# Kernel optimization log

Measured on AMD Instinct MI355X. Metric: run time of the kernel, lower is better.

Reference implementation:

```python
import jax, jax.numpy as jnp
import numpy as np

NEG_INF = 1e20  # matches INF in the torch source
EPS = 1e-12     # F.normalize default eps
THRESHOLD = 0.1  # config.graph_learn_epsilon_label2label


def setup_inputs() -> dict:
    key = jax.random.key(0)
    k1, k2, k3, k4, k5 = jax.random.split(key, 5)
    L, E, E_PT, H = 2048, 512, 300, 16
    return {
        "label_embedding": jax.random.normal(k1, (L, E), dtype=jnp.float32),
        "pretrained_label_embedding": jax.random.normal(k2, (L, E_PT), dtype=jnp.float32),
        "W_pt": jax.random.normal(k3, (H, E_PT), dtype=jnp.float32) * 0.1,
        "W_gcn0": jax.random.normal(k4, (E, E), dtype=jnp.float32) * (1.0 / np.sqrt(E)),
        "W_gcn1": jax.random.normal(k5, (E, E), dtype=jnp.float32) * (1.0 / np.sqrt(E)),
    }


def _weighted_cosine(input_pt, W_pt):
    # W_pt: [H, E_pt]; input_pt: [L, E_pt]
    w2 = W_pt ** 2                                  # [H, E_pt]
    h = input_pt[None, :, :] * w2[:, None, :]       # [H, L, E_pt]
    norm = jnp.linalg.norm(h, axis=-1, keepdims=True)
    h_norm = h / jnp.maximum(norm, EPS)             # F.normalize(p=2, dim=-1)
    # mean over heads of per-head cosine similarity: [L, L]
    scores = jnp.einsum("hle,hme->hlm", h_norm, h_norm).mean(axis=0)
    return scores


def reference(label_embedding, pretrained_label_embedding, W_pt, W_gcn0, W_gcn1):
    # 1) metric-based graph structure learning
    scores_cosine = _weighted_cosine(pretrained_label_embedding, W_pt)
    scores = jnp.where(scores_cosine >= THRESHOLD, scores_cosine, -NEG_INF)
    adj = jax.nn.softmax(scores, axis=-1)           # [L, L]

    # 2) 2-layer GCN message passing (bias=None, batch_norm=False, eval-mode dropout)
    x = jax.nn.relu(adj @ (label_embedding @ W_gcn0))
    x = jax.nn.relu(adj @ (x @ W_gcn1))
    return x
```

## Files before the change

kernel.cpp:

```cpp
#include <hip/hip_runtime.h>
#include <hip/hip_bf16.h>


typedef __attribute__((ext_vector_type(8))) short bf16x8;
typedef __attribute__((ext_vector_type(4))) float f32x4;
typedef __attribute__((ext_vector_type(4))) int i32x4;

#define L_DIM 2048
#define EPT 300
#define H_DIM 16
#define KDIM 4800
#define WINDOW 3.0e-3f

__global__ __launch_bounds__(256) void compute_y_kernel(const float* __restrict__ xpt,
                                                        const float* __restrict__ Wpt,
                                                        signed char* __restrict__ Y,
                                                        float* __restrict__ norms,
                                                        float* __restrict__ inv_s) {
  __shared__ float redmax[4];
  const int i = blockIdx.x;
  const int lane = threadIdx.x & 63;
  const int w = threadIdx.x >> 6;
  const float* x = xpt + i * EPT;
  float y[4][5];
  float wmax = 0.f;
#pragma unroll
  for (int hh = 0; hh < 4; ++hh) {
    const int h = w * 4 + hh;
    const float* wp = Wpt + h * EPT;
    float ss = 0.f;
#pragma unroll
    for (int t = 0; t < 5; ++t) {
      int e = lane + 64 * t;
      float val = 0.f;
      if (e < EPT) {
        float we = wp[e];
        val = x[e] * we * we;
      }
      y[hh][t] = val;
      ss += val * val;
    }
#pragma unroll
    for (int o = 32; o >= 1; o >>= 1) ss += __shfl_xor(ss, o, 64);
    float n = fmaxf(sqrtf(ss), 1e-12f);
    if (lane == 0) norms[i * H_DIM + h] = n;
    float scale = 0.25f / n;
#pragma unroll
    for (int t = 0; t < 5; ++t) {
      y[hh][t] *= scale;
      wmax = fmaxf(wmax, fabsf(y[hh][t]));
    }
  }
#pragma unroll
  for (int o = 32; o >= 1; o >>= 1) wmax = fmaxf(wmax, __shfl_xor(wmax, o, 64));
  if (lane == 0) redmax[w] = wmax;
  __syncthreads();
  float rowmax = fmaxf(fmaxf(redmax[0], redmax[1]), fmaxf(redmax[2], redmax[3]));
  rowmax = fmaxf(rowmax, 1e-12f);
  const float qs = 127.0f / rowmax;
  if (threadIdx.x == 0) inv_s[i] = rowmax * (1.0f / 127.0f);
#pragma unroll
  for (int hh = 0; hh < 4; ++hh) {
    const int h = w * 4 + hh;
#pragma unroll
    for (int t = 0; t < 5; ++t) {
      int e = lane + 64 * t;
      if (e < EPT) {
        int qv = __float2int_rn(y[hh][t] * qs);
        qv = max(-127, min(127, qv));
        Y[(size_t)i * KDIM + h * EPT + e] = (signed char)qv;
      }
    }
  }
}

__global__ __launch_bounds__(256) void gram_i8(const signed char* __restrict__ Y,
                                               float* __restrict__ S,
                                               const float* __restrict__ inv_s) {
  const int id = blockIdx.x;
  const int bx = (id & 7) | (((id >> 3) & 3) << 3);
  const int by = id >> 5;
  const int row0 = by * 64, col0 = bx * 64;
  if (col0 + 64 <= row0) return;
  const bool do_mirror = (col0 > row0);
  __shared__ __attribute__((aligned(16))) signed char As[4][4096];
  __shared__ __attribute__((aligned(16))) signed char Bs[4][4096];
  const int tid = threadIdx.x;
  const int lane = tid & 63;
  const int wn = tid >> 6;
  const int r = lane & 15, q = lane >> 4;
  const int srow = tid >> 2;
  const int sc = (tid & 3) ^ ((srow >> 2) & 3);

  i32x4 acc[4];
#pragma unroll
  for (int t = 0; t < 4; ++t) {
    i32x4 z = {0, 0, 0, 0};
    acc[t] = z;
  }
  const int niter = KDIM / 64;

#define STAGEI(bufi, k0)                                                                       \
  {                                                                                            \
    __builtin_amdgcn_global_load_lds(                                                          \
        (const __attribute__((address_space(1))) void*)(Y + (size_t)(row0 + srow) * KDIM +     \
                                                        (k0) + sc * 16),                       \
        (__attribute__((address_space(3))) void*)(&As[bufi][tid * 16]), 16, 0, 0);             \
    __builtin_amdgcn_global_load_lds(                                                          \
        (const __attribute__((address_space(1))) void*)(Y + (size_t)(col0 + srow) * KDIM +     \
                                                        (k0) + sc * 16),                       \
        (__attribute__((address_space(3))) void*)(&Bs[bufi][tid * 16]), 16, 0, 0);             \
  }

  auto compute = [&](int bufi) {
    const signed char* as = As[bufi];
    const signed char* bs = Bs[bufi];
    const int ch = (q ^ ((r >> 2) & 3)) * 16;
    i32x4 bfrag = *(const i32x4*)(bs + (wn * 16 + r) * 64 + ch);
#pragma unroll
    for (int t = 0; t < 4; ++t) {
      i32x4 afrag = *(const i32x4*)(as + (t * 16 + r) * 64 + ch);
      acc[t] = __builtin_amdgcn_mfma_i32_16x16x64_i8(afrag, bfrag, acc[t], 0, 0, 0);
    }
  };

  STAGEI(0, 0)
  STAGEI(1, 64)
  STAGEI(2, 128)
  for (int k = 0; k < niter - 3; ++k) {
    asm volatile("s_waitcnt vmcnt(4)" ::: "memory");
    __builtin_amdgcn_s_barrier();
    __builtin_amdgcn_sched_barrier(0);
    STAGEI((k + 3) & 3, (k + 3) * 64)
    compute(k & 3);
  }
  asm volatile("s_waitcnt vmcnt(4)" ::: "memory");
  __builtin_amdgcn_s_barrier();
  __builtin_amdgcn_sched_barrier(0);
  compute((niter - 3) & 3);
  asm volatile("s_waitcnt vmcnt(2)" ::: "memory");
  __builtin_amdgcn_s_barrier();
  __builtin_amdgcn_sched_barrier(0);
  compute((niter - 2) & 3);
  asm volatile("s_waitcnt vmcnt(0)" ::: "memory");
  __builtin_amdgcn_s_barrier();
  __builtin_amdgcn_sched_barrier(0);
  compute((niter - 1) & 3);
#undef STAGEI
  const int gc = col0 + wn * 16 + r;
  const float sj = inv_s[gc];
#pragma unroll
  for (int t = 0; t < 4; ++t) {
    int gr0 = row0 + t * 16 + q * 4;
#pragma unroll
    for (int p = 0; p < 4; ++p) {
      float vv = (float)acc[t][p] * (inv_s[gr0 + p] * sj);
      S[(size_t)(gr0 + p) * L_DIM + gc] = vv;
      if (do_mirror) S[(size_t)gc * L_DIM + (gr0 + p)] = vv;
    }
  }
}

template <int BM, int BN, bool RELU, bool OUT_BF16, bool MIRROR, bool SPLITX>
__global__ __launch_bounds__(256) void gemm_bt(const __hip_bfloat16* __restrict__ A,
                                               const __hip_bfloat16* __restrict__ B,
                                               void* __restrict__ C0v, void* __restrict__ C1v,
                                               int M, int N, int K) {
  constexpr int WMG = BM / 64;
  constexpr int WNG = 4 / WMG;
  constexpr int NC = BN / (16 * WNG);
  int bx = blockIdx.x;
  int kbeg = 0, kend = K;
  if (SPLITX) {
    const int xhalf = gridDim.x >> 1;
    const int khalf = ((K >> 1) + 63) & ~63;
    if (bx >= xhalf) {
      bx -= xhalf;
      kbeg = khalf;
    } else {
      kend = khalf;
    }
  }
  const int row0 = blockIdx.y * BM, col0 = bx * BN;
  if (MIRROR && col0 + BN <= row0) return;
  const bool do_mirror = MIRROR && (col0 > row0);
  __shared__ __attribute__((aligned(16))) __hip_bfloat16 As[2][BM * 64];
  __shared__ __attribute__((aligned(16))) __hip_bfloat16 Bs[2][BN * 64];
  const int tid = threadIdx.x;
  const int lane = tid & 63;
  const int wave = tid >> 6;
  const int wm = wave / WNG, wn = wave % WNG;
  const int r = lane & 15, q = lane >> 4;
  const int srow = tid >> 3;
  const int schunk = (tid & 7) ^ (srow & 7);

  f32x4 acc[4][NC];
#pragma unroll
  for (int a = 0; a < 4; ++a)
#pragma unroll
    for (int b = 0; b < NC; ++b) {
      f32x4 z = {0.f, 0.f, 0.f, 0.f};
      acc[a][b] = z;
    }

  const int niter = (kend - kbeg) >> 6;

#define STAGE(bufi, k0)                                                                       \
  {                                                                                           \
    _Pragma("unroll") for (int it = 0; it < BM / 32; ++it) {                                  \
      __builtin_amdgcn_global_load_lds(                                                       \
          (const __attribute__((address_space(1))) void*)(A + (size_t)(row0 + it * 32 + srow) * K + \
                                                          (k0) + schunk * 8),                 \
          (__attribute__((address_space(3))) void*)(&As[bufi][(it * 256 + tid) * 8]), 16, 0, 0); \
    }                                                                                         \
    _Pragma("unroll") for (int it = 0; it < BN / 32; ++it) {                                  \
      __builtin_amdgcn_global_load_lds(                                                       \
          (const __attribute__((address_space(1))) void*)(B + (size_t)(col0 + it * 32 + srow) * K + \
                                                          (k0) + schunk * 8),                 \
          (__attribute__((address_space(3))) void*)(&Bs[bufi][(it * 256 + tid) * 8]), 16, 0, 0); \
    }                                                                                         \
  }

  STAGE(0, kbeg)
  for (int k = 0; k < niter; ++k) {
    __syncthreads();
    if (k + 1 < niter) STAGE((k + 1) & 1, kbeg + ((k + 1) << 6))
    const __hip_bfloat16* as = As[k & 1];
    const __hip_bfloat16* bs = Bs[k & 1];
#pragma unroll
    for (int kk = 0; kk < 2; ++kk) {
      const int ch = ((kk * 4 + q) ^ (r & 7)) * 8;
      bf16x8 af[4], bfr[NC];
#pragma unroll
      for (int t = 0; t < 4; ++t)
        af[t] = *(const bf16x8*)(as + (wm * 64 + t * 16 + r) * 64 + ch);
#pragma unroll
      for (int c = 0; c < NC; ++c)
        bfr[c] = *(const bf16x8*)(bs + (wn * 16 * NC + c * 16 + r) * 64 + ch);
#pragma unroll
      for (int tm = 0; tm < 4; ++tm)
#pragma unroll
        for (int tn = 0; tn < NC; ++tn)
          acc[tm][tn] = __builtin_amdgcn_mfma_f32_16x16x32_bf16(af[tm], bfr[tn], acc[tm][tn], 0, 0, 0);
    }
  }
#undef STAGE
  float* dst = (float*)(SPLITX ? (kbeg > 0 ? C1v : C0v) : C0v);
#pragma unroll
  for (int tm = 0; tm < 4; ++tm) {
    int gr0 = row0 + wm * 64 + tm * 16 + q * 4;
#pragma unroll
    for (int tn = 0; tn < NC; ++tn) {
      int gc = col0 + wn * 16 * NC + tn * 16 + r;
#pragma unroll
      for (int p = 0; p < 4; ++p) {
        float vv = acc[tm][tn][p];
        if (RELU) vv = fmaxf(vv, 0.f);
        if (OUT_BF16) {
          ((__hip_bfloat16*)C0v)[(size_t)(gr0 + p) * N + gc] = __float2bfloat16(vv);
        } else {
          dst[(size_t)(gr0 + p) * N + gc] = vv;
          if (do_mirror) dst[(size_t)gc * N + (gr0 + p)] = vv;
        }
      }
    }
  }
}

__global__ __launch_bounds__(256) void scan_repair(float* __restrict__ S,
                                                   const float* __restrict__ xpt,
                                                   const float* __restrict__ Wpt,
                                                   const float* __restrict__ norms) {
  __shared__ int lqueue[2048];
  __shared__ int lcount;
  __shared__ float W4[KDIM];
  if (threadIdx.x == 0) lcount = 0;
  __syncthreads();
  const int row = blockIdx.x;
  const int base_idx = row * 2048;
#pragma unroll
  for (int t = 0; t < 2; ++t) {
    int col = t * 1024 + threadIdx.x * 4;
    if (col + 4 <= row) continue;
    float4 v = *(const float4*)(S + base_idx + col);
    float vv[4] = {v.x, v.y, v.z, v.w};
#pragma unroll
    for (int u = 0; u < 4; ++u) {
      int j = col + u;
      if (j >= row && fabsf(vv[u] - 0.1f) < WINDOW) {
        int p = atomicAdd(&lcount, 1);
        if (p < 2048) lqueue[p] = j;
      }
    }
  }
  __syncthreads();
  const int n = min(lcount, 2048);
  if (n == 0) return;
  for (int e = threadIdx.x; e < KDIM; e += 256) {
    float w = Wpt[e];
    float w2 = w * w;
    W4[e] = w2 * w2;
  }
  __syncthreads();
  const int lane = threadIdx.x & 63;
  const int wave = threadIdx.x >> 6;
  const int i = row;
  float xiv[5];
  {
    const float* xi = xpt + i * EPT;
#pragma unroll
    for (int t = 0; t < 5; ++t) {
      int idx = lane + 64 * t;
      xiv[t] = idx < EPT ? xi[idx] : 0.f;
    }
  }
  for (int k = wave; k < n; k += 4) {
    int j = lqueue[k];
    const float* xj = xpt + j * EPT;
    float pre[5];
#pragma unroll
    for (int t = 0; t < 5; ++t) {
      int idx = lane + 64 * t;
      pre[t] = idx < EPT ? xiv[t] * xj[idx] : 0.f;
    }
    float accv = 0.f;
#pragma unroll
    for (int h = 0; h < H_DIM; ++h) {
      float ph = 0.f;
#pragma unroll
      for (int t = 0; t < 5; ++t) {
        int idx = lane + 64 * t;
        if (idx < EPT) ph += pre[t] * W4[h * EPT + idx];
      }
      accv += ph * (1.f / (norms[i * H_DIM + h] * norms[j * H_DIM + h]));
    }
#pragma unroll
    for (int o = 32; o >= 1; o >>= 1) accv += __shfl_xor(accv, o, 64);
    if (lane == 0) {
      float val = accv * (1.f / 16.f);
      S[(size_t)i * L_DIM + j] = val;
      S[(size_t)j * L_DIM + i] = val;
    }
  }
}

__global__ __launch_bounds__(256) void post_kernel(const float* __restrict__ S,
                                                   __hip_bfloat16* __restrict__ adj,
                                                   const float* __restrict__ label,
                                                   __hip_bfloat16* __restrict__ Lbf,
                                                   const float* __restrict__ W0,
                                                   const float* __restrict__ W1,
                                                   __hip_bfloat16* __restrict__ W0t,
                                                   __hip_bfloat16* __restrict__ W1t) {
  __shared__ float red[4];
  __shared__ float tile[32][33];
  const int b = blockIdx.x;
  const int tid = threadIdx.x;
  if (b < 2048) {
    const int row = b;
    const float* s = S + (size_t)row * L_DIM;
    float m = -1e30f;
    for (int j = tid; j < L_DIM; j += 256) {
      float v = s[j];
      if (v >= 0.1f && v > m) m = v;
    }
#pragma unroll
    for (int o = 32; o >= 1; o >>= 1) m = fmaxf(m, __shfl_xor(m, o, 64));
    if ((tid & 63) == 0) red[tid >> 6] = m;
    __syncthreads();
    m = fmaxf(fmaxf(red[0], red[1]), fmaxf(red[2], red[3]));
    float sum = 0.f;
    for (int j = tid; j < L_DIM; j += 256) {
      float v = s[j];
      if (v >= 0.1f) sum += __expf(v - m);
    }
#pragma unroll
    for (int o = 32; o >= 1; o >>= 1) sum += __shfl_xor(sum, o, 64);
    __syncthreads();
    if ((tid & 63) == 0) red[tid >> 6] = sum;
    __syncthreads();
    sum = red[0] + red[1] + red[2] + red[3];
    float inv = 1.f / sum;
    for (int j = tid; j < L_DIM; j += 256) {
      float v = s[j];
      float a = (v >= 0.1f) ? __expf(v - m) * inv : 0.f;
      adj[(size_t)row * L_DIM + j] = __float2bfloat16(a);
    }
    return;
  }
  if (b < 6144) {
    int i = (b - 2048) * 256 + tid;
    Lbf[i] = __float2bfloat16(label[i]);
    return;
  }
  int local = b - 6144;
  const bool first = local < 256;
  const float* src = first ? W0 : W1;
  __hip_bfloat16* dst = first ? W0t : W1t;
  int rem = local & 255;
  int c0 = (rem & 15) * 32, r0 = (rem >> 4) * 32;
  int tx = tid & 31, ty = tid >> 5;
  for (int i2 = ty; i2 < 32; i2 += 8) tile[i2][tx] = src[(size_t)(r0 + i2) * 512 + c0 + tx];
  __syncthreads();
  for (int i2 = ty; i2 < 32; i2 += 8)
    dst[(size_t)(c0 + i2) * 512 + r0 + tx] = __float2bfloat16(tile[tx][i2]);
}

__global__ void combine_relu_bf16(const float* __restrict__ P0, const float* __restrict__ P1,
                                  __hip_bfloat16* __restrict__ X) {
  int i = blockIdx.x * 256 + threadIdx.x;
  float4 a = ((const float4*)P0)[i];
  float4 b = ((const float4*)P1)[i];
  __hip_bfloat16 o0 = __float2bfloat16(fmaxf(a.x + b.x, 0.f));
  __hip_bfloat16 o1 = __float2bfloat16(fmaxf(a.y + b.y, 0.f));
  __hip_bfloat16 o2 = __float2bfloat16(fmaxf(a.z + b.z, 0.f));
  __hip_bfloat16 o3 = __float2bfloat16(fmaxf(a.w + b.w, 0.f));
  X[4 * i + 0] = o0;
  X[4 * i + 1] = o1;
  X[4 * i + 2] = o2;
  X[4 * i + 3] = o3;
}

__global__ void combine_relu_f32(const float* __restrict__ P0, const float* __restrict__ P1,
                                 float* __restrict__ X) {
  int i = blockIdx.x * 256 + threadIdx.x;
  float4 a = ((const float4*)P0)[i];
  float4 b = ((const float4*)P1)[i];
  float4 v;
  v.x = fmaxf(a.x + b.x, 0.f);
  v.y = fmaxf(a.y + b.y, 0.f);
  v.z = fmaxf(a.z + b.z, 0.f);
  v.w = fmaxf(a.w + b.w, 0.f);
  ((float4*)X)[i] = v;
}

extern "C" void kernel_launch(void* const* d_in, const int* in_sizes, int n_in, void* d_out,
                              int out_size, void* d_ws, size_t ws_size, hipStream_t stream) {
  const float* label = (const float*)d_in[0];
  const float* xpt = (const float*)d_in[1];
  const float* Wpt = (const float*)d_in[2];
  const float* W0 = (const float*)d_in[3];
  const float* W1 = (const float*)d_in[4];
  float* out = (float*)d_out;

  char* ws = (char*)d_ws;
  signed char* Y = (signed char*)ws;
  float* S = (float*)(ws + 19660800);
  float* norms = (float*)(ws + 36438016);
  float* P0 = (float*)(ws + 36569088);
  float* P1 = (float*)(ws + 40763392);
  float* inv_s = (float*)(ws + 44957696);
  __hip_bfloat16* adj = (__hip_bfloat16*)ws;
  __hip_bfloat16* Lbf = (__hip_bfloat16*)(ws + 8388608);
  __hip_bfloat16* W0t = (__hip_bfloat16*)(ws + 10485760);
  __hip_bfloat16* W1t = (__hip_bfloat16*)(ws + 11010048);
  __hip_bfloat16* T0t = (__hip_bfloat16*)(ws + 11534336);
  __hip_bfloat16* X1 = (__hip_bfloat16*)(ws + 13631488);
  __hip_bfloat16* T1t = (__hip_bfloat16*)(ws + 15728640);

  compute_y_kernel<<<2048, 256, 0, stream>>>(xpt, Wpt, Y, norms, inv_s);
  gram_i8<<<1024, 256, 0, stream>>>(Y, S, inv_s);
  scan_repair<<<2048, 256, 0, stream>>>(S, xpt, Wpt, norms);
  post_kernel<<<6656, 256, 0, stream>>>(S, adj, label, Lbf, W0, W1, W0t, W1t);
  gemm_bt<64, 64, false, true, false, false><<<dim3(32, 8), 256, 0, stream>>>(W0t, Lbf, T0t, nullptr, 512, 2048, 512);
  gemm_bt<64, 64, false, false, false, true><<<dim3(16, 32), 256, 0, stream>>>(adj, T0t, P0, P1, 2048, 512, 2048);
  combine_relu_bf16<<<1024, 256, 0, stream>>>(P0, P1, X1);
  gemm_bt<64, 64, false, true, false, false><<<dim3(32, 8), 256, 0, stream>>>(W1t, X1, T1t, nullptr, 512, 2048, 512);
  gemm_bt<64, 64, false, false, false, true><<<dim3(16, 32), 256, 0, stream>>>(adj, T1t, P0, P1, 2048, 512, 2048);
  combine_relu_f32<<<1024, 256, 0, stream>>>(P0, P1, out);
}
```

Before: 204.5 us.

## Fuse prep, repair and softmax kernels; drop split-K GEMMs and combine passes

The bf16 casts and weight transposes move into the Y-quantization kernel. The first projection GEMM (W0t x Lbf) now runs on the otherwise idle lower-triangle blocks of the int8 Gram kernel. The near-threshold repair scan merges with the softmax row kernel, which stages the row in LDS and recomputes borderline entries locally instead of writing them back to S. The adjacency GEMMs drop split-K and the separate combine_relu kernels, applying ReLU in-kernel with fewer blocks, which trades parallelism for fewer launches and less traffic.

After: 225.8 us. 10.4% more time.

```diff
diff --git a/kernel.cpp b/kernel.cpp
--- a/kernel.cpp
+++ b/kernel.cpp
@@ -12,83 +12,175 @@
 #define KDIM 4800
 #define WINDOW 3.0e-3f
 
-__global__ __launch_bounds__(256) void compute_y_kernel(const float* __restrict__ xpt,
-                                                        const float* __restrict__ Wpt,
-                                                        signed char* __restrict__ Y,
-                                                        float* __restrict__ norms,
-                                                        float* __restrict__ inv_s) {
+__global__ __launch_bounds__(256) void prep_kernel(const float* __restrict__ xpt,
+                                                   const float* __restrict__ Wpt,
+                                                   const float* __restrict__ label,
+                                                   const float* __restrict__ W0,
+                                                   const float* __restrict__ W1,
+                                                   signed char* __restrict__ Y,
+                                                   float* __restrict__ norms,
+                                                   float* __restrict__ inv_s,
+                                                   __hip_bfloat16* __restrict__ Lbf,
+                                                   __hip_bfloat16* __restrict__ W0t,
+                                                   __hip_bfloat16* __restrict__ W1t) {
   __shared__ float redmax[4];
-  const int i = blockIdx.x;
-  const int lane = threadIdx.x & 63;
-  const int w = threadIdx.x >> 6;
-  const float* x = xpt + i * EPT;
-  float y[4][5];
-  float wmax = 0.f;
-#pragma unroll
-  for (int hh = 0; hh < 4; ++hh) {
-    const int h = w * 4 + hh;
-    const float* wp = Wpt + h * EPT;
-    float ss = 0.f;
-#pragma unroll
-    for (int t = 0; t < 5; ++t) {
-      int e = lane + 64 * t;
-      float val = 0.f;
-      if (e < EPT) {
-        float we = wp[e];
-        val = x[e] * we * we;
-      }
-      y[hh][t] = val;
-      ss += val * val;
-    }
-#pragma unroll
-    for (int o = 32; o >= 1; o >>= 1) ss += __shfl_xor(ss, o, 64);
-    float n = fmaxf(sqrtf(ss), 1e-12f);
-    if (lane == 0) norms[i * H_DIM + h] = n;
-    float scale = 0.25f / n;
-#pragma unroll
-    for (int t = 0; t < 5; ++t) {
-      y[hh][t] *= scale;
-      wmax = fmaxf(wmax, fabsf(y[hh][t]));
-    }
-  }
-#pragma unroll
-  for (int o = 32; o >= 1; o >>= 1) wmax = fmaxf(wmax, __shfl_xor(wmax, o, 64));
-  if (lane == 0) redmax[w] = wmax;
-  __syncthreads();
-  float rowmax = fmaxf(fmaxf(redmax[0], redmax[1]), fmaxf(redmax[2], redmax[3]));
-  rowmax = fmaxf(rowmax, 1e-12f);
-  const float qs = 127.0f / rowmax;
-  if (threadIdx.x == 0) inv_s[i] = rowmax * (1.0f / 127.0f);
-#pragma unroll
-  for (int hh = 0; hh < 4; ++hh) {
-    const int h = w * 4 + hh;
-#pragma unroll
-    for (int t = 0; t < 5; ++t) {
-      int e = lane + 64 * t;
-      if (e < EPT) {
-        int qv = __float2int_rn(y[hh][t] * qs);
-        qv = max(-127, min(127, qv));
-        Y[(size_t)i * KDIM + h * EPT + e] = (signed char)qv;
-      }
-    }
-  }
+  __shared__ float tile[32][33];
+  const int b = blockIdx.x;
+  const int tid = threadIdx.x;
+  if (b < 2048) {
+    const int i = b;
+    const int lane = tid & 63;
+    const int w = tid >> 6;
+    const float* x = xpt + i * EPT;
+    float y[4][5];
+    float wmax = 0.f;
+#pragma unroll
+    for (int hh = 0; hh < 4; ++hh) {
+      const int h = w * 4 + hh;
+      const float* wp = Wpt + h * EPT;
+      float ss = 0.f;
+#pragma unroll
+      for (int t = 0; t < 5; ++t) {
+        int e = lane + 64 * t;
+        float val = 0.f;
+        if (e < EPT) {
+          float we = wp[e];
+          val = x[e] * we * we;
+        }
+        y[hh][t] = val;
+        ss += val * val;
+      }
+#pragma unroll
+      for (int o = 32; o >= 1; o >>= 1) ss += __shfl_xor(ss, o, 64);
+      float n = fmaxf(sqrtf(ss), 1e-12f);
+      if (lane == 0) norms[i * H_DIM + h] = n;
+      float scale = 0.25f / n;
+#pragma unroll
+      for (int t = 0; t < 5; ++t) {
+        y[hh][t] *= scale;
+        wmax = fmaxf(wmax, fabsf(y[hh][t]));
+      }
+    }
+#pragma unroll
+    for (int o = 32; o >= 1; o >>= 1) wmax = fmaxf(wmax, __shfl_xor(wmax, o, 64));
+    if (lane == 0) redmax[w] = wmax;
+    __syncthreads();
+    float rowmax = fmaxf(fmaxf(redmax[0], redmax[1]), fmaxf(redmax[2], redmax[3]));
+    rowmax = fmaxf(rowmax, 1e-12f);
+    const float qs = 127.0f / rowmax;
+    if (tid == 0) inv_s[i] = rowmax * (1.0f / 127.0f);
+#pragma unroll
+    for (int hh = 0; hh < 4; ++hh) {
+      const int h = w * 4 + hh;
+#pragma unroll
+      for (int t = 0; t < 5; ++t) {
+        int e = lane + 64 * t;
+        if (e < EPT) {
+          int qv = __float2int_rn(y[hh][t] * qs);
+          qv = max(-127, min(127, qv));
+          Y[(size_t)i * KDIM + h * EPT + e] = (signed char)qv;
+        }
+      }
+    }
+    return;
+  }
+  if (b < 6144) {
+    int i = (b - 2048) * 256 + tid;
+    Lbf[i] = __float2bfloat16(label[i]);
+    return;
+  }
+  int local = b - 6144;
+  const bool first = local < 256;
+  const float* src = first ? W0 : W1;
+  __hip_bfloat16* dst = first ? W0t : W1t;
+  int rem = local & 255;
+  int c0 = (rem & 15) * 32, r0 = (rem >> 4) * 32;
+  int tx = tid & 31, ty = tid >> 5;
+  for (int i2 = ty; i2 < 32; i2 += 8) tile[i2][tx] = src[(size_t)(r0 + i2) * 512 + c0 + tx];
+  __syncthreads();
+  for (int i2 = ty; i2 < 32; i2 += 8)
+    dst[(size_t)(c0 + i2) * 512 + r0 + tx] = __float2bfloat16(tile[tx][i2]);
 }
 
 __global__ __launch_bounds__(256) void gram_i8(const signed char* __restrict__ Y,
                                                float* __restrict__ S,
-                                               const float* __restrict__ inv_s) {
+                                               const float* __restrict__ inv_s,
+                                               const __hip_bfloat16* __restrict__ W0t,
+                                               const __hip_bfloat16* __restrict__ Lbf,
+                                               __hip_bfloat16* __restrict__ T0t) {
+  __shared__ __attribute__((aligned(16))) char smem[32768];
   const int id = blockIdx.x;
   const int bx = (id & 7) | (((id >> 3) & 3) << 3);
   const int by = id >> 5;
   const int row0 = by * 64, col0 = bx * 64;
-  if (col0 + 64 <= row0) return;
-  const bool do_mirror = (col0 > row0);
-  __shared__ __attribute__((aligned(16))) signed char As[4][4096];
-  __shared__ __attribute__((aligned(16))) signed char Bs[4][4096];
   const int tid = threadIdx.x;
   const int lane = tid & 63;
   const int wn = tid >> 6;
   const int r = lane & 15, q = lane >> 4;
+
+  if (col0 + 64 <= row0) {
+    const int d = (by * (by - 1)) / 2 + bx;
+    if (d >= 256) return;
+    const int row0r = (d >> 5) * 64;
+    const int col0r = (d & 31) * 64;
+    __hip_bfloat16* Asb = (__hip_bfloat16*)smem;
+    __hip_bfloat16* Bsb = (__hip_bfloat16*)(smem + 16384);
+    const int srow8 = tid >> 3;
+    const int schunk8 = (tid & 7) ^ (srow8 & 7);
+    f32x4 racc[4];
+#pragma unroll
+    for (int t = 0; t < 4; ++t) {
+      f32x4 z = {0.f, 0.f, 0.f, 0.f};
+      racc[t] = z;
+    }
+#define RSTAGE(bufi, k0)                                                                      \
+  {                                                                                           \
+    _Pragma("unroll") for (int it = 0; it < 2; ++it) {                                        \
+      __builtin_amdgcn_global_load_lds(                                                       \
+          (const __attribute__((address_space(1))) void*)(W0t + (size_t)(row0r + it * 32 + srow8) * 512 + \
+                                                          (k0) + schunk8 * 8),                \
+          (__attribute__((address_space(3))) void*)(Asb + (bufi)*4096 + (it * 256 + tid) * 8), 16, 0, 0); \
+    }                                                                                         \
+    _Pragma("unroll") for (int it = 0; it < 2; ++it) {                                        \
+      __builtin_amdgcn_global_load_lds(                                                       \
+          (const __attribute__((address_space(1))) void*)(Lbf + (size_t)(col0r + it * 32 + srow8) * 512 + \
+                                                          (k0) + schunk8 * 8),                \
+          (__attribute__((address_space(3))) void*)(Bsb + (bufi)*4096 + (it * 256 + tid) * 8), 16, 0, 0); \
+    }                                                                                         \
+  }
+    RSTAGE(0, 0)
+    for (int k = 0; k < 8; ++k) {
+      __syncthreads();
+      if (k + 1 < 8) RSTAGE((k + 1) & 1, (k + 1) * 64)
+      const __hip_bfloat16* as = Asb + (k & 1) * 4096;
+      const __hip_bfloat16* bs = Bsb + (k & 1) * 4096;
+#pragma unroll
+      for (int kk = 0; kk < 2; ++kk) {
+        const int ch = ((kk * 4 + q) ^ (r & 7)) * 8;
+        bf16x8 af[4];
+#pragma unroll
+        for (int t = 0; t < 4; ++t) af[t] = *(const bf16x8*)(as + (t * 16 + r) * 64 + ch);
+        bf16x8 bfr = *(const bf16x8*)(bs + (wn * 16 + r) * 64 + ch);
+#pragma unroll
+        for (int t = 0; t < 4; ++t)
+          racc[t] = __builtin_amdgcn_mfma_f32_16x16x32_bf16(af[t], bfr, racc[t], 0, 0, 0);
+      }
+    }
+#undef RSTAGE
+    const int gcr = col0r + wn * 16 + r;
+#pragma unroll
+    for (int t = 0; t < 4; ++t) {
+      int gr0 = row0r + t * 16 + q * 4;
+#pragma unroll
+      for (int p = 0; p < 4; ++p)
+        T0t[(size_t)(gr0 + p) * 2048 + gcr] = __float2bfloat16(racc[t][p]);
+    }
+    return;
+  }
+
+  const bool do_mirror = (col0 > row0);
+  signed char* As = (signed char*)smem;
+  signed char* Bs = (signed char*)(smem + 16384);
   const int srow = tid >> 2;
   const int sc = (tid & 3) ^ ((srow >> 2) & 3);
 
@@ -105,16 +197,16 @@
     __builtin_amdgcn_global_load_lds(                                                          \
         (const __attribute__((address_space(1))) void*)(Y + (size_t)(row0 + srow) * KDIM +     \
                                                         (k0) + sc * 16),                       \
-        (__attribute__((address_space(3))) void*)(&As[bufi][tid * 16]), 16, 0, 0);             \
+        (__attribute__((address_space(3))) void*)(As + (bufi)*4096 + tid * 16), 16, 0, 0);     \
     __builtin_amdgcn_global_load_lds(                                                          \
         (const __attribute__((address_space(1))) void*)(Y + (size_t)(col0 + srow) * KDIM +     \
                                                         (k0) + sc * 16),                       \
-        (__attribute__((address_space(3))) void*)(&Bs[bufi][tid * 16]), 16, 0, 0);             \
+        (__attribute__((address_space(3))) void*)(Bs + (bufi)*4096 + tid * 16), 16, 0, 0);     \
   }
 
   auto compute = [&](int bufi) {
-    const signed char* as = As[bufi];
-    const signed char* bs = Bs[bufi];
+    const signed char* as = As + bufi * 4096;
+    const signed char* bs = Bs + bufi * 4096;
     const int ch = (q ^ ((r >> 2) & 3)) * 16;
     i32x4 bfrag = *(const i32x4*)(bs + (wn * 16 + r) * 64 + ch);
 #pragma unroll
@@ -161,29 +253,15 @@
   }
 }
 
-template <int BM, int BN, bool RELU, bool OUT_BF16, bool MIRROR, bool SPLITX>
+template <int BM, int BN, bool RELU, bool OUT_BF16>
 __global__ __launch_bounds__(256) void gemm_bt(const __hip_bfloat16* __restrict__ A,
                                                const __hip_bfloat16* __restrict__ B,
-                                               void* __restrict__ C0v, void* __restrict__ C1v,
+                                               void* __restrict__ C0v,
                                                int M, int N, int K) {
   constexpr int WMG = BM / 64;
   constexpr int WNG = 4 / WMG;
   constexpr int NC = BN / (16 * WNG);
-  int bx = blockIdx.x;
-  int kbeg = 0, kend = K;
-  if (SPLITX) {
-    const int xhalf = gridDim.x >> 1;
-    const int khalf = ((K >> 1) + 63) & ~63;
-    if (bx >= xhalf) {
-      bx -= xhalf;
-      kbeg = khalf;
-    } else {
-      kend = khalf;
-    }
-  }
-  const int row0 = blockIdx.y * BM, col0 = bx * BN;
-  if (MIRROR && col0 + BN <= row0) return;
-  const bool do_mirror = MIRROR && (col0 > row0);
+  const int row0 = blockIdx.y * BM, col0 = blockIdx.x * BN;
   __shared__ __attribute__((aligned(16))) __hip_bfloat16 As[2][BM * 64];
   __shared__ __attribute__((aligned(16))) __hip_bfloat16 Bs[2][BN * 64];
   const int tid = threadIdx.x;
@@ -203,7 +281,7 @@
       acc[a][b] = z;
     }
 
-  const int niter = (kend - kbeg) >> 6;
+  const int niter = K >> 6;
 
 #define STAGE(bufi, k0)                                                                       \
   {                                                                                           \
@@ -221,10 +299,10 @@
     }                                                                                         \
   }
 
-  STAGE(0, kbeg)
+  STAGE(0, 0)
   for (int k = 0; k < niter; ++k) {
     __syncthreads();
-    if (k + 1 < niter) STAGE((k + 1) & 1, kbeg + ((k + 1) << 6))
+    if (k + 1 < niter) STAGE((k + 1) & 1, (k + 1) << 6)
     const __hip_bfloat16* as = As[k & 1];
     const __hip_bfloat16* bs = Bs[k & 1];
 #pragma unroll
@@ -245,7 +323,6 @@
     }
   }
 #undef STAGE
-  float* dst = (float*)(SPLITX ? (kbeg > 0 ? C1v : C0v) : C0v);
 #pragma unroll
   for (int tm = 0; tm < 4; ++tm) {
     int gr0 = row0 + wm * 64 + tm * 16 + q * 4;
@@ -259,179 +336,113 @@
         if (OUT_BF16) {
           ((__hip_bfloat16*)C0v)[(size_t)(gr0 + p) * N + gc] = __float2bfloat16(vv);
         } else {
-          dst[(size_t)(gr0 + p) * N + gc] = vv;
-          if (do_mirror) dst[(size_t)gc * N + (gr0 + p)] = vv;
+          ((float*)C0v)[(size_t)(gr0 + p) * N + gc] = vv;
         }
       }
     }
   }
 }
 
-__global__ __launch_bounds__(256) void scan_repair(float* __restrict__ S,
+__global__ __launch_bounds__(256) void post_kernel(const float* __restrict__ S,
+                                                   __hip_bfloat16* __restrict__ adj,
                                                    const float* __restrict__ xpt,
                                                    const float* __restrict__ Wpt,
                                                    const float* __restrict__ norms) {
-  __shared__ int lqueue[2048];
+  __shared__ float rowv[L_DIM];
+  __shared__ float W4[KDIM];
+  __shared__ int lq[2048];
   __shared__ int lcount;
-  __shared__ float W4[KDIM];
-  if (threadIdx.x == 0) lcount = 0;
-  __syncthreads();
-  const int row = blockIdx.x;
-  const int base_idx = row * 2048;
-#pragma unroll
-  for (int t = 0; t < 2; ++t) {
-    int col = t * 1024 + threadIdx.x * 4;
-    if (col + 4 <= row) continue;
-    float4 v = *(const float4*)(S + base_idx + col);
+  __shared__ float red[4];
+  const int b = blockIdx.x;
+  const int tid = threadIdx.x;
+  if (tid == 0) lcount = 0;
+  __syncthreads();
+  const float* s = S + (size_t)b * L_DIM;
+  for (int j0 = tid * 4; j0 < L_DIM; j0 += 1024) {
+    float4 v = *(const float4*)(s + j0);
+    *(float4*)(&rowv[j0]) = v;
     float vv[4] = {v.x, v.y, v.z, v.w};
 #pragma unroll
     for (int u = 0; u < 4; ++u) {
-      int j = col + u;
-      if (j >= row && fabsf(vv[u] - 0.1f) < WINDOW) {
+      if (fabsf(vv[u] - 0.1f) < WINDOW) {
         int p = atomicAdd(&lcount, 1);
-        if (p < 2048) lqueue[p] = j;
-      }
-    }
-  }
-  __syncthreads();
-  const int n = min(lcount, 2048);
-  if (n == 0) return;
-  for (int e = threadIdx.x; e < KDIM; e += 256) {
-    float w = Wpt[e];
-    float w2 = w * w;
-    W4[e] = w2 * w2;
-  }
-  __syncthreads();
-  const int lane = threadIdx.x & 63;
-  const int wave = threadIdx.x >> 6;
-  const int i = row;
-  float xiv[5];
-  {
-    const float* xi = xpt + i * EPT;
-#pragma unroll
-    for (int t = 0; t < 5; ++t) {
-      int idx = lane + 64 * t;
-      xiv[t] = idx < EPT ? xi[idx] : 0.f;
-    }
-  }
-  for (int k = wave; k < n; k += 4) {
-    int j = lqueue[k];
-    const float* xj = xpt + j * EPT;
-    float pre[5];
-#pragma unroll
-    for (int t = 0; t < 5; ++t) {
-      int idx = lane + 64 * t;
-      pre[t] = idx < EPT ? xiv[t] * xj[idx] : 0.f;
-    }
-    float accv = 0.f;
-#pragma unroll
-    for (int h = 0; h < H_DIM; ++h) {
-      float ph = 0.f;
+        lq[p] = j0 + u;
+      }
+    }
+  }
+  __syncthreads();
+  const int n = lcount;
+  if (n > 0) {
+    for (int e = tid; e < KDIM; e += 256) {
+      float w = Wpt[e];
+      float w2 = w * w;
+      W4[e] = w2 * w2;
+    }
+    __syncthreads();
+    const int lane = tid & 63;
+    const int wave = tid >> 6;
+    float xiv[5];
+    {
+      const float* xi = xpt + b * EPT;
 #pragma unroll
       for (int t = 0; t < 5; ++t) {
         int idx = lane + 64 * t;
-        if (idx < EPT) ph += pre[t] * W4[h * EPT + idx];
-      }
-      accv += ph * (1.f / (norms[i * H_DIM + h] * norms[j * H_DIM + h]));
-    }
-#pragma unroll
-    for (int o = 32; o >= 1; o >>= 1) accv += __shfl_xor(accv, o, 64);
-    if (lane == 0) {
-      float val = accv * (1.f / 16.f);
-      S[(size_t)i * L_DIM + j] = val;
-      S[(size_t)j * L_DIM + i] = val;
-    }
-  }
-}
-
-__global__ __launch_bounds__(256) void post_kernel(const float* __restrict__ S,
-                                                   __hip_bfloat16* __restrict__ adj,
-                                                   const float* __restrict__ label,
-                                                   __hip_bfloat16* __restrict__ Lbf,
-                                                   const float* __restrict__ W0,
-                                                   const float* __restrict__ W1,
-                                                   __hip_bfloat16* __restrict__ W0t,
-                                                   __hip_bfloat16* __restrict__ W1t) {
-  __shared__ float red[4];
-  __shared__ float tile[32][33];
-  const int b = blockIdx.x;
-  const int tid = threadIdx.x;
-  if (b < 2048) {
-    const int row = b;
-    const float* s = S + (size_t)row * L_DIM;
-    float m = -1e30f;
-    for (int j = tid; j < L_DIM; j += 256) {
-      float v = s[j];
-      if (v >= 0.1f && v > m) m = v;
-    }
-#pragma unroll
-    for (int o = 32; o >= 1; o >>= 1) m = fmaxf(m, __shfl_xor(m, o, 64));
-    if ((tid & 63) == 0) red[tid >> 6] = m;
+        xiv[t] = idx < EPT ? xi[idx] : 0.f;
+      }
+    }
+    for (int k = wave; k < n; k += 4) {
+      int j = lq[k];
+      const float* xj = xpt + j * EPT;
+      float pre[5];
+#pragma unroll
+      for (int t = 0; t < 5; ++t) {
+        int idx = lane + 64 * t;
+        pre[t] = idx < EPT ? xiv[t] * xj[idx] : 0.f;
+      }
+      float accv = 0.f;
+#pragma unroll
+      for (int h = 0; h < H_DIM; ++h) {
+        float ph = 0.f;
+#pragma unroll
+        for (int t = 0; t < 5; ++t) {
+          int idx = lane + 64 * t;
+          if (idx < EPT) ph += pre[t] * W4[h * EPT + idx];
+        }
+        accv += ph * (1.f / (norms[b * H_DIM + h] * norms[j * H_DIM + h]));
+      }
+#pragma unroll
+      for (int o = 32; o >= 1; o >>= 1) accv += __shfl_xor(accv, o, 64);
+      if (lane == 0) rowv[j] = accv * (1.f / 16.f);
+    }
     __syncthreads();
-    m = fmaxf(fmaxf(red[0], red[1]), fmaxf(red[2], red[3]));
-    float sum = 0.f;
-    for (int j = tid; j < L_DIM; j += 256) {
-      float v = s[j];
-      if (v >= 0.1f) sum += __expf(v - m);
-    }
-#pragma unroll
-    for (int o = 32; o >= 1; o >>= 1) sum += __shfl_xor(sum, o, 64);
-    __syncthreads();
-    if ((tid & 63) == 0) red[tid >> 6] = sum;
-    __syncthreads();
-    sum = red[0] + red[1] + red[2] + red[3];
-    float inv = 1.f / sum;
-    for (int j = tid; j < L_DIM; j += 256) {
-      float v = s[j];
-      float a = (v >= 0.1f) ? __expf(v - m) * inv : 0.f;
-      adj[(size_t)row * L_DIM + j] = __float2bfloat16(a);
-    }
-    return;
-  }
-  if (b < 6144) {
-    int i = (b - 2048) * 256 + tid;
-    Lbf[i] = __float2bfloat16(label[i]);
-    return;
-  }
-  int local = b - 6144;
-  const bool first = local < 256;
-  const float* src = first ? W0 : W1;
-  __hip_bfloat16* dst = first ? W0t : W1t;
-  int rem = local & 255;
-  int c0 = (rem & 15) * 32, r0 = (rem >> 4) * 32;
-  int tx = tid & 31, ty = tid >> 5;
-  for (int i2 = ty; i2 < 32; i2 += 8) tile[i2][tx] = src[(size_t)(r0 + i2) * 512 + c0 + tx];
-  __syncthreads();
-  for (int i2 = ty; i2 < 32; i2 += 8)
-    dst[(size_t)(c0 + i2) * 512 + r0 + tx] = __float2bfloat16(tile[tx][i2]);
-}
-
-__global__ void combine_relu_bf16(const float* __restrict__ P0, const float* __restrict__ P1,
-                                  __hip_bfloat16* __restrict__ X) {
-  int i = blockIdx.x * 256 + threadIdx.x;
-  float4 a = ((const float4*)P0)[i];
-  float4 b = ((const float4*)P1)[i];
-  __hip_bfloat16 o0 = __float2bfloat16(fmaxf(a.x + b.x, 0.f));
-  __hip_bfloat16 o1 = __float2bfloat16(fmaxf(a.y + b.y, 0.f));
-  __hip_bfloat16 o2 = __float2bfloat16(fmaxf(a.z + b.z, 0.f));
-  __hip_bfloat16 o3 = __float2bfloat16(fmaxf(a.w + b.w, 0.f));
-  X[4 * i + 0] = o0;
-  X[4 * i + 1] = o1;
-  X[4 * i + 2] = o2;
-  X[4 * i + 3] = o3;
-}
-
-__global__ void combine_relu_f32(const float* __restrict__ P0, const float* __restrict__ P1,
-                                 float* __restrict__ X) {
-  int i = blockIdx.x * 256 + threadIdx.x;
-  float4 a = ((const float4*)P0)[i];
-  float4 b = ((const float4*)P1)[i];
-  float4 v;
-  v.x = fmaxf(a.x + b.x, 0.f);
-  v.y = fmaxf(a.y + b.y, 0.f);
-  v.z = fmaxf(a.z + b.z, 0.f);
-  v.w = fmaxf(a.w + b.w, 0.f);
-  ((float4*)X)[i] = v;
+  }
+  float m = -1e30f;
+  for (int j = tid; j < L_DIM; j += 256) {
+    float v = rowv[j];
+    if (v >= 0.1f && v > m) m = v;
+  }
+#pragma unroll
+  for (int o = 32; o >= 1; o >>= 1) m = fmaxf(m, __shfl_xor(m, o, 64));
+  if ((tid & 63) == 0) red[tid >> 6] = m;
+  __syncthreads();
+  m = fmaxf(fmaxf(red[0], red[1]), fmaxf(red[2], red[3]));
+  float sum = 0.f;
+  for (int j = tid; j < L_DIM; j += 256) {
+    float v = rowv[j];
+    if (v >= 0.1f) sum += __expf(v - m);
+  }
+#pragma unroll
+  for (int o = 32; o >= 1; o >>= 1) sum += __shfl_xor(sum, o, 64);
+  __syncthreads();
+  if ((tid & 63) == 0) red[tid >> 6] = sum;
+  __syncthreads();
+  sum = red[0] + red[1] + red[2] + red[3];
+  float inv = 1.f / sum;
+  for (int j = tid; j < L_DIM; j += 256) {
+    float v = rowv[j];
+    float a = (v >= 0.1f) ? __expf(v - m) * inv : 0.f;
+    adj[(size_t)b * L_DIM + j] = __float2bfloat16(a);
+  }
 }
 
 extern "C" void kernel_launch(void* const* d_in, const int* in_sizes, int n_in, void* d_out,
@@ -447,25 +458,19 @@
   signed char* Y = (signed char*)ws;
   float* S = (float*)(ws + 19660800);
   float* norms = (float*)(ws + 36438016);
-  float* P0 = (float*)(ws + 36569088);
-  float* P1 = (float*)(ws + 40763392);
   float* inv_s = (float*)(ws + 44957696);
+  __hip_bfloat16* Lbf = (__hip_bfloat16*)(ws + 44965888);
   __hip_bfloat16* adj = (__hip_bfloat16*)ws;
-  __hip_bfloat16* Lbf = (__hip_bfloat16*)(ws + 8388608);
   __hip_bfloat16* W0t = (__hip_bfloat16*)(ws + 10485760);
   __hip_bfloat16* W1t = (__hip_bfloat16*)(ws + 11010048);
   __hip_bfloat16* T0t = (__hip_bfloat16*)(ws + 11534336);
   __hip_bfloat16* X1 = (__hip_bfloat16*)(ws + 13631488);
   __hip_bfloat16* T1t = (__hip_bfloat16*)(ws + 15728640);
 
-  compute_y_kernel<<<2048, 256, 0, stream>>>(xpt, Wpt, Y, norms, inv_s);
-  gram_i8<<<1024, 256, 0, stream>>>(Y, S, inv_s);
-  scan_repair<<<2048, 256, 0, stream>>>(S, xpt, Wpt, norms);
-  post_kernel<<<6656, 256, 0, stream>>>(S, adj, label, Lbf, W0, W1, W0t, W1t);
-  gemm_bt<64, 64, false, true, false, false><<<dim3(32, 8), 256, 0, stream>>>(W0t, Lbf, T0t, nullptr, 512, 2048, 512);
-  gemm_bt<64, 64, false, false, false, true><<<dim3(16, 32), 256, 0, stream>>>(adj, T0t, P0, P1, 2048, 512, 2048);
-  combine_relu_bf16<<<1024, 256, 0, stream>>>(P0, P1, X1);
-  gemm_bt<64, 64, false, true, false, false><<<dim3(32, 8), 256, 0, stream>>>(W1t, X1, T1t, nullptr, 512, 2048, 512);
-  gemm_bt<64, 64, false, false, false, true><<<dim3(16, 32), 256, 0, stream>>>(adj, T1t, P0, P1, 2048, 512, 2048);
-  combine_relu_f32<<<1024, 256, 0, stream>>>(P0, P1, out);
+  prep_kernel<<<6656, 256, 0, stream>>>(xpt, Wpt, label, W0, W1, Y, norms, inv_s, Lbf, W0t, W1t);
+  gram_i8<<<1024, 256, 0, stream>>>(Y, S, inv_s, W0t, Lbf, T0t);
+  post_kernel<<<2048, 256, 0, stream>>>(S, adj, xpt, Wpt, norms);
+  gemm_bt<64, 64, true, true><<<dim3(8, 32), 256, 0, stream>>>(adj, T0t, X1, 2048, 512, 2048);
+  gemm_bt<64, 64, false, true><<<dim3(32, 8), 256, 0, stream>>>(W1t, X1, T1t, 512, 2048, 512);
+  gemm_bt<64, 64, true, false><<<dim3(8, 32), 256, 0, stream>>>(adj, T1t, out, 2048, 512, 2048);
 }
```
